# Kernel tuning notes

Measured on AMD Instinct MI355X. Metric: run time of the kernel, lower is better.

Reference implementation:

```python
import jax, jax.numpy as jnp
import numpy as np
from jax import lax

N = 4194304
DELTA_T = 1.0
ETA = 1.0
QN = 1.5 * 3600.0
INITIAL_X2 = 1.0


def setup_inputs() -> dict:
    key = jax.random.key(0)
    k1, k2, k3 = jax.random.split(key, 3)
    return {
        "uk_sequence": jax.random.normal(k1, (N,), dtype=jnp.float32),
        "Rp": jnp.float32(1.0),
        "Cp": jnp.float32(1.0),
        "R0": jax.random.uniform(k2, (), dtype=jnp.float32),
        "a_coeffs": jax.random.normal(k3, (9,), dtype=jnp.float32) * 0.1,
    }


def _forward(uk_sequence, Rp, Cp, R0, a_coeffs):
    # Diagonal linear SSM, state = (x1, x2)
    A00 = jnp.exp(-DELTA_T / (Rp * Cp))            # decay of RC branch
    B0 = Rp * (1.0 - A00)                           # input gain on x1
    B1 = jnp.float32(-ETA * DELTA_T / QN)           # constant coulomb-counting gain

    def step(carry, u):
        x1, x2 = carry
        nxt = (A00 * x1 + B0 * u, x2 + B1 * u)
        return nxt, carry                           # emit state BEFORE update (xk[k])

    init = (jnp.float32(0.0), jnp.float32(INITIAL_X2))
    _, (x1s, x2s) = lax.scan(step, init, uk_sequence)  # each [N]

    # poly8(x2) = a0 + a1*x2 + ... + a8*x2^8 via Horner (highest-first for polyval)
    poly = jnp.polyval(a_coeffs[::-1], x2s)
    y = poly - x1s - R0 * uk_sequence               # [N]
    return y[:, None]                               # [N, 1] to match torch output


def reference(uk_sequence, Rp, Cp, R0, a_coeffs):
    return _forward(uk_sequence, Rp, Cp, R0, a_coeffs)
```

## Files before the change

### kernel.cpp

```cpp
#include <hip/hip_runtime.h>


constexpr int BLOCK = 256;
constexpr int TPER  = 16;
constexpr int CHUNK = BLOCK * TPER;
constexpr int NTOT  = 4194304;
constexpr int NB    = NTOT / CHUNK;
constexpr int WPB   = BLOCK / 64;
constexpr int APT   = NB / BLOCK;

__global__ __launch_bounds__(BLOCK) void kA_agg(
    const float* __restrict__ u,
    const float* __restrict__ Rp_p, const float* __restrict__ Cp_p,
    float* __restrict__ aggW, float* __restrict__ aggP)
{
    __shared__ float LW[WPB], LP[WPB];
    const int b = blockIdx.x, t = threadIdx.x;
    const int lane = t & 63, w = t >> 6;

    const float invRC = 1.0f / (Rp_p[0] * Cp_p[0]);
    const float A00 = __expf(-invRC);
    const float a2 = A00 * A00, a4 = a2 * a2, a8 = a4 * a4;
    const float f16 = a8 * a8;

    const float4* up = (const float4*)(u + (size_t)b * CHUNK + (size_t)t * TPER);
    float4 v[4];
    v[0] = up[0]; v[1] = up[1]; v[2] = up[2]; v[3] = up[3];
    const float* uu = (const float*)v;

    float s = 0.0f, p = 0.0f;
#pragma unroll
    for (int i = 0; i < TPER; ++i) { s = fmaf(A00, s, uu[i]); p += uu[i]; }

    float fk = f16;
#pragma unroll
    for (int k = 1; k < 64; k <<= 1) {
        const float sw = __shfl_up(s, k, 64);
        const float pw = __shfl_up(p, k, 64);
        if (lane >= k) { s = fmaf(sw, fk, s); p += pw; }
        fk *= fk;
    }
    if (lane == 63) { LW[w] = s; LP[w] = p; }
    __syncthreads();

    if (t == 0) {
        float f1024 = f16;
        for (int i = 0; i < 6; ++i) f1024 *= f1024;
        float W = LW[0], P = LP[0];
        for (int q = 1; q < WPB; ++q) { W = fmaf(W, f1024, LW[q]); P += LP[q]; }
        aggW[b] = W; aggP[b] = P;
    }
}

__global__ __launch_bounds__(BLOCK) void kB_emit(
    const float* __restrict__ u,
    const float* __restrict__ Rp_p, const float* __restrict__ Cp_p,
    const float* __restrict__ R0_p, const float* __restrict__ ac,
    const float* __restrict__ aggW, const float* __restrict__ aggP,
    float* __restrict__ out)
{
    __shared__ float LW[WPB], LP[WPB];
    __shared__ float sRed[WPB];
    __shared__ float sCW;

    const int b = blockIdx.x, t = threadIdx.x;
    const int lane = t & 63, w = t >> 6;

    const float invRC = 1.0f / (Rp_p[0] * Cp_p[0]);
    const float A00 = __expf(-invRC);
    const float B0  = Rp_p[0] * (1.0f - A00);
    const float B1  = -1.0f / 5400.0f;
    const float R0f = R0_p[0];
    const float a2 = A00 * A00, a4 = a2 * a2, a8 = a4 * a4;
    const float f16 = a8 * a8;
    float f1024 = f16;
    for (int i = 0; i < 6; ++i) f1024 *= f1024;
    const float dC = (f1024 * f1024) * (f1024 * f1024);

    const size_t base = (size_t)b * CHUNK + (size_t)t * TPER;
    const float4* up = (const float4*)(u + base);
    float4 v[4];
    v[0] = up[0]; v[1] = up[1]; v[2] = up[2]; v[3] = up[3];
    const float* uu = (const float*)v;

    float pc = 0.0f;
#pragma unroll
    for (int i = 0; i < APT; ++i) {
        const int j = t * APT + i;
        if (j < b) pc += aggP[j];
    }
#pragma unroll
    for (int off = 32; off; off >>= 1) pc += __shfl_down(pc, off, 64);
    if (lane == 0) sRed[w] = pc;

    if (t == 0) {
        float cW;
        if (dC == 0.0f) {
            cW = (b > 0) ? aggW[b - 1] : 0.0f;
        } else {
            cW = 0.0f;
            for (int j = 0; j < b; ++j) cW = fmaf(cW, dC, aggW[j]);
        }
        sCW = cW;
    }

    float s = 0.0f, p = 0.0f;
#pragma unroll
    for (int i = 0; i < TPER; ++i) { s = fmaf(A00, s, uu[i]); p += uu[i]; }
    float fk = f16;
#pragma unroll
    for (int k = 1; k < 64; k <<= 1) {
        const float sw = __shfl_up(s, k, 64);
        const float pw = __shfl_up(p, k, 64);
        if (lane >= k) { s = fmaf(sw, fk, s); p += pw; }
        fk *= fk;
    }
    if (lane == 63) { LW[w] = s; LP[w] = p; }
    __syncthreads();

    float carryP_blk = 0.0f;
#pragma unroll
    for (int q = 0; q < WPB; ++q) carryP_blk += sRed[q];

    float cw = 0.0f, cp = 0.0f;
    for (int q = 0; q < w; ++q) { cw = fmaf(cw, f1024, LW[q]); cp += LP[q]; }

    float fw = 1.0f;
    for (int q = 0; q < w; ++q) fw *= f1024;

    float fl = 1.0f, bse = f16;
#pragma unroll
    for (int k = 0; k < 6; ++k) { if (lane & (1 << k)) fl *= bse; bse *= bse; }

    const float upW = __shfl_up(s, 1, 64);
    const float upP = __shfl_up(p, 1, 64);
    float Wcur = (lane ? upW : 0.0f) + fmaf(sCW, fw, cw) * fl;
    float Pcur = (lane ? upP : 0.0f) + cp + carryP_blk;

    float af[9];
#pragma unroll
    for (int i = 0; i < 9; ++i) af[i] = ac[i];

    float4 o[4];
    float* oy = (float*)o;
#pragma unroll
    for (int i = 0; i < TPER; ++i) {
        const float x2 = fmaf(B1, Pcur, 1.0f);
        float poly = af[8];
#pragma unroll
        for (int j = 7; j >= 0; --j) poly = fmaf(poly, x2, af[j]);
        oy[i] = poly - B0 * Wcur - R0f * uu[i];
        Wcur = fmaf(A00, Wcur, uu[i]);
        Pcur += uu[i];
    }
    float4* op = (float4*)(out + base);
    op[0] = o[0]; op[1] = o[1]; op[2] = o[2]; op[3] = o[3];
}

extern "C" void kernel_launch(void* const* d_in, const int* in_sizes, int n_in,
                              void* d_out, int out_size, void* d_ws, size_t ws_size,
                              hipStream_t stream) {
    const float* u    = (const float*)d_in[0];
    const float* Rp_p = (const float*)d_in[1];
    const float* Cp_p = (const float*)d_in[2];
    const float* R0_p = (const float*)d_in[3];
    const float* ac   = (const float*)d_in[4];
    float* out = (float*)d_out;

    float* wsW = (float*)d_ws;
    float* wsP = (float*)d_ws + NB;

    kA_agg <<<NB, BLOCK, 0, stream>>>(u, Rp_p, Cp_p, wsW, wsP);
    kB_emit<<<NB, BLOCK, 0, stream>>>(u, Rp_p, Cp_p, R0_p, ac, wsW, wsP, out);
}
```

Before: 84.32 us.

## Fuse scan aggregate and emit kernels into one cooperative launch with grid sync

```diff
diff --git a/kernel.cpp b/kernel.cpp
--- a/kernel.cpp
+++ b/kernel.cpp
@@ -1,4 +1,7 @@
 #include <hip/hip_runtime.h>
+#include <hip/hip_cooperative_groups.h>
+
+namespace cg = cooperative_groups;
 
 
 constexpr int BLOCK = 256;
@@ -8,6 +11,128 @@
 constexpr int NB    = NTOT / CHUNK;
 constexpr int WPB   = BLOCK / 64;
 constexpr int APT   = NB / BLOCK;
+
+__global__ __launch_bounds__(BLOCK, 4) void k_fused(
+    const float* __restrict__ u,
+    const float* __restrict__ Rp_p, const float* __restrict__ Cp_p,
+    const float* __restrict__ R0_p, const float* __restrict__ ac,
+    float* __restrict__ aggW, float* __restrict__ aggP,
+    float* __restrict__ out)
+{
+    __shared__ float LW[WPB], LP[WPB];
+    __shared__ float sRed[WPB];
+    __shared__ float sCW;
+
+    const int b = blockIdx.x, t = threadIdx.x;
+    const int lane = t & 63, w = t >> 6;
+
+    const float Rp  = Rp_p[0];
+    const float invRC = 1.0f / (Rp * Cp_p[0]);
+    const float A00 = __expf(-invRC);
+    const float B0  = Rp * (1.0f - A00);
+    const float B1  = -1.0f / 5400.0f;
+    const float a2 = A00 * A00, a4 = a2 * a2, a8 = a4 * a4;
+    const float f16 = a8 * a8;
+    float f1024 = f16;
+    for (int i = 0; i < 6; ++i) f1024 *= f1024;
+    const float dC = (f1024 * f1024) * (f1024 * f1024);
+
+    const size_t base = (size_t)b * CHUNK + (size_t)t * TPER;
+    const float4* up = (const float4*)(u + base);
+    float4 v[4];
+    v[0] = up[0]; v[1] = up[1]; v[2] = up[2]; v[3] = up[3];
+    const float* uu = (const float*)v;
+
+    float s = 0.0f, p = 0.0f;
+#pragma unroll
+    for (int i = 0; i < TPER; ++i) { s = fmaf(A00, s, uu[i]); p += uu[i]; }
+
+    float fk = f16;
+#pragma unroll
+    for (int k = 1; k < 64; k <<= 1) {
+        const float sw = __shfl_up(s, k, 64);
+        const float pw = __shfl_up(p, k, 64);
+        if (lane >= k) { s = fmaf(sw, fk, s); p += pw; }
+        fk *= fk;
+    }
+    if (lane == 63) { LW[w] = s; LP[w] = p; }
+    __syncthreads();
+
+    if (t == 0) {
+        float W = LW[0], P = LP[0];
+        for (int q = 1; q < WPB; ++q) { W = fmaf(W, f1024, LW[q]); P += LP[q]; }
+        __hip_atomic_store(&aggW[b], W, __ATOMIC_RELAXED, __HIP_MEMORY_SCOPE_AGENT);
+        __hip_atomic_store(&aggP[b], P, __ATOMIC_RELAXED, __HIP_MEMORY_SCOPE_AGENT);
+    }
+
+    cg::this_grid().sync();
+
+    float pc = 0.0f;
+#pragma unroll
+    for (int i = 0; i < APT; ++i) {
+        const int j = t * APT + i;
+        if (j < b)
+            pc += __hip_atomic_load(&aggP[j], __ATOMIC_RELAXED, __HIP_MEMORY_SCOPE_AGENT);
+    }
+#pragma unroll
+    for (int off = 32; off; off >>= 1) pc += __shfl_down(pc, off, 64);
+    if (lane == 0) sRed[w] = pc;
+
+    if (t == 0) {
+        float cW;
+        if (dC == 0.0f) {
+            cW = (b > 0) ? __hip_atomic_load(&aggW[b - 1], __ATOMIC_RELAXED,
+                                             __HIP_MEMORY_SCOPE_AGENT)
+                         : 0.0f;
+        } else {
+            cW = 0.0f;
+            for (int j = 0; j < b; ++j)
+                cW = fmaf(cW, dC, __hip_atomic_load(&aggW[j], __ATOMIC_RELAXED,
+                                                    __HIP_MEMORY_SCOPE_AGENT));
+        }
+        sCW = cW;
+    }
+    __syncthreads();
+
+    float carryP_blk = 0.0f;
+#pragma unroll
+    for (int q = 0; q < WPB; ++q) carryP_blk += sRed[q];
+
+    float cw = 0.0f, cp = 0.0f;
+    for (int q = 0; q < w; ++q) { cw = fmaf(cw, f1024, LW[q]); cp += LP[q]; }
+
+    float fw = 1.0f;
+    for (int q = 0; q < w; ++q) fw *= f1024;
+
+    float fl = 1.0f, bse = f16;
+#pragma unroll
+    for (int k = 0; k < 6; ++k) { if (lane & (1 << k)) fl *= bse; bse *= bse; }
+
+    const float upW = __shfl_up(s, 1, 64);
+    const float upP = __shfl_up(p, 1, 64);
+    float Wcur = (lane ? upW : 0.0f) + fmaf(sCW, fw, cw) * fl;
+    float Pcur = (lane ? upP : 0.0f) + cp + carryP_blk;
+
+    const float R0f = R0_p[0];
+    float af[9];
+#pragma unroll
+    for (int i = 0; i < 9; ++i) af[i] = ac[i];
+
+    float4 o[4];
+    float* oy = (float*)o;
+#pragma unroll
+    for (int i = 0; i < TPER; ++i) {
+        const float x2 = fmaf(B1, Pcur, 1.0f);
+        float poly = af[8];
+#pragma unroll
+        for (int j = 7; j >= 0; --j) poly = fmaf(poly, x2, af[j]);
+        oy[i] = poly - B0 * Wcur - R0f * uu[i];
+        Wcur = fmaf(A00, Wcur, uu[i]);
+        Pcur += uu[i];
+    }
+    float4* op = (float4*)(out + base);
+    op[0] = o[0]; op[1] = o[1]; op[2] = o[2]; op[3] = o[3];
+}
 
 __global__ __launch_bounds__(BLOCK) void kA_agg(
     const float* __restrict__ u,
@@ -170,6 +295,12 @@
     float* wsW = (float*)d_ws;
     float* wsP = (float*)d_ws + NB;
 
-    kA_agg <<<NB, BLOCK, 0, stream>>>(u, Rp_p, Cp_p, wsW, wsP);
-    kB_emit<<<NB, BLOCK, 0, stream>>>(u, Rp_p, Cp_p, R0_p, ac, wsW, wsP, out);
+    void* args[] = {(void*)&u, (void*)&Rp_p, (void*)&Cp_p, (void*)&R0_p,
+                    (void*)&ac, (void*)&wsW, (void*)&wsP, (void*)&out};
+    hipError_t err = hipLaunchCooperativeKernel((const void*)k_fused, dim3(NB),
+                                                dim3(BLOCK), args, 0, stream);
+    if (err != hipSuccess) {
+        kA_agg <<<NB, BLOCK, 0, stream>>>(u, Rp_p, Cp_p, wsW, wsP);
+        kB_emit<<<NB, BLOCK, 0, stream>>>(u, Rp_p, Cp_p, R0_p, ac, wsW, wsP, out);
+    }
 }
```

After: 212.6 us. +152.2%, slower.

## Fuse two-pass scan into single kernel with decoupled flag-based block lookback

Applied to the files above, without the earlier changes.

```diff
diff --git a/kernel.cpp b/kernel.cpp
--- a/kernel.cpp
+++ b/kernel.cpp
@@ -9,21 +9,37 @@
 constexpr int WPB   = BLOCK / 64;
 constexpr int APT   = NB / BLOCK;
 
-__global__ __launch_bounds__(BLOCK) void kA_agg(
+constexpr unsigned MAGIC1 = 0x1B7F3A55u;
+constexpr unsigned MAGIC2 = 0x9C24E16Bu;
+
+__global__ __launch_bounds__(BLOCK, 4) void k_scan(
     const float* __restrict__ u,
     const float* __restrict__ Rp_p, const float* __restrict__ Cp_p,
-    float* __restrict__ aggW, float* __restrict__ aggP)
+    const float* __restrict__ R0_p, const float* __restrict__ ac,
+    float* __restrict__ aggW, float* __restrict__ aggP,
+    unsigned* __restrict__ flagA, unsigned* __restrict__ flagB,
+    float* __restrict__ out)
 {
     __shared__ float LW[WPB], LP[WPB];
+    __shared__ float sRed[WPB];
+    __shared__ float sCW;
+
     const int b = blockIdx.x, t = threadIdx.x;
     const int lane = t & 63, w = t >> 6;
 
-    const float invRC = 1.0f / (Rp_p[0] * Cp_p[0]);
+    const float Rp  = Rp_p[0];
+    const float invRC = 1.0f / (Rp * Cp_p[0]);
     const float A00 = __expf(-invRC);
+    const float B0  = Rp * (1.0f - A00);
+    const float B1  = -1.0f / 5400.0f;
     const float a2 = A00 * A00, a4 = a2 * a2, a8 = a4 * a4;
     const float f16 = a8 * a8;
+    float f1024 = f16;
+    for (int i = 0; i < 6; ++i) f1024 *= f1024;
+    const float dC = (f1024 * f1024) * (f1024 * f1024);
 
-    const float4* up = (const float4*)(u + (size_t)b * CHUNK + (size_t)t * TPER);
+    const size_t base = (size_t)b * CHUNK + (size_t)t * TPER;
+    const float4* up = (const float4*)(u + base);
     float4 v[4];
     v[0] = up[0]; v[1] = up[1]; v[2] = up[2]; v[3] = up[3];
     const float* uu = (const float*)v;
@@ -44,78 +60,62 @@
     __syncthreads();
 
     if (t == 0) {
-        float f1024 = f16;
-        for (int i = 0; i < 6; ++i) f1024 *= f1024;
         float W = LW[0], P = LP[0];
         for (int q = 1; q < WPB; ++q) { W = fmaf(W, f1024, LW[q]); P += LP[q]; }
-        aggW[b] = W; aggP[b] = P;
+        __hip_atomic_store(&aggW[b], W, __ATOMIC_RELAXED, __HIP_MEMORY_SCOPE_AGENT);
+        __hip_atomic_store(&aggP[b], P, __ATOMIC_RELAXED, __HIP_MEMORY_SCOPE_AGENT);
+        __hip_atomic_store(&flagA[b], MAGIC1 ^ (unsigned)b,
+                           __ATOMIC_RELEASE, __HIP_MEMORY_SCOPE_AGENT);
+        __hip_atomic_store(&flagB[b], MAGIC2 + (unsigned)b,
+                           __ATOMIC_RELEASE, __HIP_MEMORY_SCOPE_AGENT);
     }
-}
-
-__global__ __launch_bounds__(BLOCK) void kB_emit(
-    const float* __restrict__ u,
-    const float* __restrict__ Rp_p, const float* __restrict__ Cp_p,
-    const float* __restrict__ R0_p, const float* __restrict__ ac,
-    const float* __restrict__ aggW, const float* __restrict__ aggP,
-    float* __restrict__ out)
-{
-    __shared__ float LW[WPB], LP[WPB];
-    __shared__ float sRed[WPB];
-    __shared__ float sCW;
-
-    const int b = blockIdx.x, t = threadIdx.x;
-    const int lane = t & 63, w = t >> 6;
-
-    const float invRC = 1.0f / (Rp_p[0] * Cp_p[0]);
-    const float A00 = __expf(-invRC);
-    const float B0  = Rp_p[0] * (1.0f - A00);
-    const float B1  = -1.0f / 5400.0f;
-    const float R0f = R0_p[0];
-    const float a2 = A00 * A00, a4 = a2 * a2, a8 = a4 * a4;
-    const float f16 = a8 * a8;
-    float f1024 = f16;
-    for (int i = 0; i < 6; ++i) f1024 *= f1024;
-    const float dC = (f1024 * f1024) * (f1024 * f1024);
-
-    const size_t base = (size_t)b * CHUNK + (size_t)t * TPER;
-    const float4* up = (const float4*)(u + base);
-    float4 v[4];
-    v[0] = up[0]; v[1] = up[1]; v[2] = up[2]; v[3] = up[3];
-    const float* uu = (const float*)v;
 
     float pc = 0.0f;
 #pragma unroll
     for (int i = 0; i < APT; ++i) {
         const int j = t * APT + i;
-        if (j < b) pc += aggP[j];
+        if (j < b) {
+            while (__hip_atomic_load(&flagA[j], __ATOMIC_ACQUIRE,
+                                     __HIP_MEMORY_SCOPE_AGENT) != (MAGIC1 ^ (unsigned)j))
+                __builtin_amdgcn_s_sleep(1);
+            while (__hip_atomic_load(&flagB[j], __ATOMIC_ACQUIRE,
+                                     __HIP_MEMORY_SCOPE_AGENT) != (MAGIC2 + (unsigned)j))
+                __builtin_amdgcn_s_sleep(1);
+            pc += __hip_atomic_load(&aggP[j], __ATOMIC_RELAXED, __HIP_MEMORY_SCOPE_AGENT);
+        }
     }
 #pragma unroll
     for (int off = 32; off; off >>= 1) pc += __shfl_down(pc, off, 64);
     if (lane == 0) sRed[w] = pc;
 
     if (t == 0) {
-        float cW;
-        if (dC == 0.0f) {
-            cW = (b > 0) ? aggW[b - 1] : 0.0f;
-        } else {
-            cW = 0.0f;
-            for (int j = 0; j < b; ++j) cW = fmaf(cW, dC, aggW[j]);
+        float cW = 0.0f;
+        if (b > 0) {
+            if (dC == 0.0f) {
+                const int j = b - 1;
+                while (__hip_atomic_load(&flagA[j], __ATOMIC_ACQUIRE,
+                                         __HIP_MEMORY_SCOPE_AGENT) != (MAGIC1 ^ (unsigned)j))
+                    __builtin_amdgcn_s_sleep(1);
+                while (__hip_atomic_load(&flagB[j], __ATOMIC_ACQUIRE,
+                                         __HIP_MEMORY_SCOPE_AGENT) != (MAGIC2 + (unsigned)j))
+                    __builtin_amdgcn_s_sleep(1);
+                cW = __hip_atomic_load(&aggW[j], __ATOMIC_RELAXED,
+                                       __HIP_MEMORY_SCOPE_AGENT);
+            } else {
+                for (int j = 0; j < b; ++j) {
+                    while (__hip_atomic_load(&flagA[j], __ATOMIC_ACQUIRE,
+                                             __HIP_MEMORY_SCOPE_AGENT) != (MAGIC1 ^ (unsigned)j))
+                        __builtin_amdgcn_s_sleep(1);
+                    while (__hip_atomic_load(&flagB[j], __ATOMIC_ACQUIRE,
+                                             __HIP_MEMORY_SCOPE_AGENT) != (MAGIC2 + (unsigned)j))
+                        __builtin_amdgcn_s_sleep(1);
+                    cW = fmaf(cW, dC, __hip_atomic_load(&aggW[j], __ATOMIC_RELAXED,
+                                                        __HIP_MEMORY_SCOPE_AGENT));
+                }
+            }
         }
         sCW = cW;
     }
-
-    float s = 0.0f, p = 0.0f;
-#pragma unroll
-    for (int i = 0; i < TPER; ++i) { s = fmaf(A00, s, uu[i]); p += uu[i]; }
-    float fk = f16;
-#pragma unroll
-    for (int k = 1; k < 64; k <<= 1) {
-        const float sw = __shfl_up(s, k, 64);
-        const float pw = __shfl_up(p, k, 64);
-        if (lane >= k) { s = fmaf(sw, fk, s); p += pw; }
-        fk *= fk;
-    }
-    if (lane == 63) { LW[w] = s; LP[w] = p; }
     __syncthreads();
 
     float carryP_blk = 0.0f;
@@ -137,6 +137,7 @@
     float Wcur = (lane ? upW : 0.0f) + fmaf(sCW, fw, cw) * fl;
     float Pcur = (lane ? upP : 0.0f) + cp + carryP_blk;
 
+    const float R0f = R0_p[0];
     float af[9];
 #pragma unroll
     for (int i = 0; i < 9; ++i) af[i] = ac[i];
@@ -167,9 +168,11 @@
     const float* ac   = (const float*)d_in[4];
     float* out = (float*)d_out;
 
-    float* wsW = (float*)d_ws;
-    float* wsP = (float*)d_ws + NB;
+    float*    wsW   = (float*)d_ws;
+    float*    wsP   = (float*)d_ws + NB;
+    unsigned* wsFA  = (unsigned*)((float*)d_ws + 2 * NB);
+    unsigned* wsFB  = (unsigned*)((float*)d_ws + 3 * NB);
 
-    kA_agg <<<NB, BLOCK, 0, stream>>>(u, Rp_p, Cp_p, wsW, wsP);
-    kB_emit<<<NB, BLOCK, 0, stream>>>(u, Rp_p, Cp_p, R0_p, ac, wsW, wsP, out);
+    k_scan<<<NB, BLOCK, 0, stream>>>(u, Rp_p, Cp_p, R0_p, ac,
+                                     wsW, wsP, wsFA, wsFB, out);
 }
```

Result: slower. 275.7 us (+227.0%).
